# Kernel tuning notes

Hardware: AMD Instinct MI355X
Metric: run time of the kernel (lower is better)

Reference implementation:

```python
import jax, jax.numpy as jnp
import numpy as np

N, C, H, W = 8, 256, 64, 64
Q_REDUCE, K_REDUCE, V_REDUCE = 8, 8, 1


def setup_inputs() -> dict:
    key = jax.random.key(0)
    ks = jax.random.split(key, 6)
    Cq, Ck, Cv = C // Q_REDUCE, C // K_REDUCE, C // V_REDUCE
    s = 0.02
    x = jax.random.normal(ks[0], (N, C, H, W), dtype=jnp.float32)
    Wq = jax.random.normal(ks[1], (Cq, C), dtype=jnp.float32) * s
    Wk = jax.random.normal(ks[2], (Ck, C), dtype=jnp.float32) * s
    Wv = jax.random.normal(ks[3], (Cv, C), dtype=jnp.float32) * s
    Wo = jax.random.normal(ks[4], (C, Cv), dtype=jnp.float32) * s
    gamma = jax.random.normal(ks[5], (), dtype=jnp.float32)  # trained scalar (init 0.0 in torch)
    return {"x": x, "Wq": Wq, "Wk": Wk, "Wv": Wv, "Wo": Wo, "gamma": gamma}


def reference(x, Wq, Wk, Wv, Wo, gamma):
    n, c, h, w = x.shape
    xf = x.reshape(n, c, h * w)                      # [N, C, HW]
    q = jnp.einsum('qc,ncl->nql', Wq, xf)            # [N, Cq, HW] (1x1 conv)
    k = jnp.einsum('kc,ncl->nkl', Wk, xf)            # [N, Ck, HW]
    v = jnp.einsum('vc,ncl->nvl', Wv, xf)            # [N, Cv, HW]
    e = jnp.einsum('nci,ncj->nij', q, k)             # [N, HW, HW], unscaled energies
    a = jax.nn.softmax(e, axis=-1)                   # softmax over keys j
    o = jnp.einsum('nvi,nij->nvj', v, a)             # [N, Cv, HW]  (o = bmm(v, a))
    o = o.reshape(n, -1, w, h)                       # faithful: view(N,-1,W,H)
    out = jnp.einsum('ov,nvhw->nohw', Wo, o)         # output 1x1 conv
    return gamma * out
```

## Files before the change

kernel.cpp:

```cpp
#include <hip/hip_runtime.h>
#include <hip/hip_bf16.h>

#define NB 8
#define CIN 256
#define LL 4096
#define CQ 32
#define CV 256

typedef __attribute__((ext_vector_type(8))) short bf16x8;
typedef __attribute__((ext_vector_type(4))) float f32x4;

__device__ __forceinline__ unsigned short f2bf(float f) {
    union { __hip_bfloat16 h; unsigned short u; } c;
    c.h = __float2bfloat16(f);
    return c.u;
}
__device__ __forceinline__ unsigned int f2bf2(float a, float b) {
    union { __hip_bfloat162 h; unsigned int u; } c;
    float2 f; f.x = a; f.y = b;
    c.h = __float22bfloat162_rn(f);
    return c.u;
}

__global__ __launch_bounds__(256) void k_wcast(
    const float* __restrict__ Wq, const float* __restrict__ Wk,
    const float* __restrict__ Wv, const float* __restrict__ Wo,
    unsigned short* __restrict__ Wb, unsigned short* __restrict__ Wob)
{
    const float LOG2E = 1.4426950408889634f;
    const int row = blockIdx.x, t = threadIdx.x;
    if (row < 320) {
        float val;
        if (row < 32)      val = Wq[row * 256 + t] * LOG2E;
        else if (row < 64) val = Wk[(row - 32) * 256 + t];
        else               val = Wv[(row - 64) * 256 + t];
        Wb[row * 256 + t] = f2bf(val);
    } else {
        const int r2 = row - 320;
        Wob[r2 * 256 + t] = f2bf(Wo[r2 * 256 + t]);
    }
}

__global__ __launch_bounds__(256) void k_qkv2(
    const float* __restrict__ x, const unsigned short* __restrict__ Wb,
    unsigned short* __restrict__ qkt, unsigned short* __restrict__ v)
{
    __shared__ unsigned short xlds[64][264];
    __shared__ unsigned short tr[64][72];
    const int n = blockIdx.y, l0 = blockIdx.x * 64, t = threadIdx.x;
    const int w = t >> 6, lane = t & 63, lid = lane & 15, quad = lane >> 4;

    #pragma unroll
    for (int part = 0; part < 8; part++) {
        const int cbase = part * 32 + w * 8;
        float tmp[8];
        #pragma unroll
        for (int cc = 0; cc < 8; cc++)
            tmp[cc] = x[(n * CIN + cbase + cc) * LL + l0 + lane];
        bf16x8 s;
        #pragma unroll
        for (int cc = 0; cc < 8; cc++) s[cc] = (short)f2bf(tmp[cc]);
        *(bf16x8*)&xlds[lane][cbase] = s;
    }
    __syncthreads();

    const f32x4 fzero = {0.f, 0.f, 0.f, 0.f};
    f32x4 acc[5][4];
    #pragma unroll
    for (int mt = 0; mt < 5; mt++)
        #pragma unroll
        for (int nt = 0; nt < 4; nt++) acc[mt][nt] = fzero;

    for (int k0 = 0; k0 < 256; k0 += 32) {
        bf16x8 bx[4];
        #pragma unroll
        for (int nt = 0; nt < 4; nt++)
            bx[nt] = *(const bf16x8*)&xlds[nt * 16 + lid][k0 + quad * 8];
        #pragma unroll
        for (int mt = 0; mt < 5; mt++) {
            const int row = (mt == 0) ? (w * 16 + lid) : (64 + w * 64 + (mt - 1) * 16 + lid);
            const bf16x8 wa = *(const bf16x8*)&Wb[row * 256 + k0 + quad * 8];
            #pragma unroll
            for (int nt = 0; nt < 4; nt++)
                acc[mt][nt] = __builtin_amdgcn_mfma_f32_16x16x32_bf16(wa, bx[nt], acc[mt][nt], 0, 0, 0);
        }
    }
    #pragma unroll
    for (int mt = 1; mt < 5; mt++)
        #pragma unroll
        for (int nt = 0; nt < 4; nt++)
            #pragma unroll
            for (int reg = 0; reg < 4; reg++) {
                const int vr = w * 64 + (mt - 1) * 16 + quad * 4 + reg;
                v[((size_t)n * CV + vr) * LL + l0 + nt * 16 + lid] = f2bf(acc[mt][nt][reg]);
            }
    #pragma unroll
    for (int nt = 0; nt < 4; nt++)
        #pragma unroll
        for (int reg = 0; reg < 4; reg++)
            tr[nt * 16 + lid][w * 16 + quad * 4 + reg] = f2bf(acc[0][nt][reg]);
    __syncthreads();
    {
        const int l = t >> 2, c = (t & 3) * 16;
        uint4 d0 = *(const uint4*)&tr[l][c];
        uint4 d1 = *(const uint4*)&tr[l][c + 8];
        uint4* dst = (uint4*)&qkt[((size_t)n * LL + l0 + l) * 64 + c];
        dst[0] = d0; dst[1] = d1;
    }
}

__global__ __launch_bounds__(256) void k_rowsum2(
    const unsigned short* __restrict__ qkt, float* __restrict__ lns)
{
    __shared__ float red[64];
    const int n = blockIdx.y, i0 = blockIdx.x * 64, t = threadIdx.x;
    const int w = t >> 6, lane = t & 63, lid = lane & 15, quad = lane >> 4;
    if (t < 64) red[t] = 0.f;
    __syncthreads();

    bf16x8 aq[4];
    #pragma unroll
    for (int mt = 0; mt < 4; mt++)
        aq[mt] = *(const bf16x8*)&qkt[((size_t)n * LL + i0 + mt * 16 + lid) * 64 + quad * 8];

    const f32x4 fzero = {0.f, 0.f, 0.f, 0.f};
    float sums[4][4];
    #pragma unroll
    for (int mt = 0; mt < 4; mt++)
        #pragma unroll
        for (int reg = 0; reg < 4; reg++) sums[mt][reg] = 0.f;

    for (int jt = 0; jt < 16; jt++) {
        const int j0 = jt * 256 + w * 64;
        bf16x8 bk[4];
        #pragma unroll
        for (int nt = 0; nt < 4; nt++)
            bk[nt] = *(const bf16x8*)&qkt[((size_t)n * LL + j0 + nt * 16 + lid) * 64 + 32 + quad * 8];
        #pragma unroll
        for (int mt = 0; mt < 4; mt++)
            #pragma unroll
            for (int nt = 0; nt < 4; nt++) {
                f32x4 e = __builtin_amdgcn_mfma_f32_16x16x32_bf16(aq[mt], bk[nt], fzero, 0, 0, 0);
                sums[mt][0] += __builtin_exp2f(e[0]);
                sums[mt][1] += __builtin_exp2f(e[1]);
                sums[mt][2] += __builtin_exp2f(e[2]);
                sums[mt][3] += __builtin_exp2f(e[3]);
            }
    }
    #pragma unroll
    for (int mt = 0; mt < 4; mt++)
        #pragma unroll
        for (int reg = 0; reg < 4; reg++) {
            float s = sums[mt][reg];
            s += __shfl_xor(s, 1); s += __shfl_xor(s, 2);
            s += __shfl_xor(s, 4); s += __shfl_xor(s, 8);
            if (lid == 0) atomicAdd(&red[mt * 16 + quad * 4 + reg], s);
        }
    __syncthreads();
    if (t < 64) lns[n * LL + i0 + t] = -__builtin_log2f(red[t]);
}

__device__ __forceinline__ void write_p(unsigned short (*pl)[64], const f32x4* e,
                                        int w, int lid, int quad, int xkey)
{
    #pragma unroll
    for (int nt = 0; nt < 4; nt++) {
        const unsigned a01 = f2bf2(__builtin_exp2f(e[nt][0]), __builtin_exp2f(e[nt][1]));
        const unsigned a23 = f2bf2(__builtin_exp2f(e[nt][2]), __builtin_exp2f(e[nt][3]));
        const int chunk = (2 * w + (quad >> 1)) ^ xkey;
        unsigned* p = (unsigned*)&pl[nt * 16 + lid][chunk * 8 + (quad & 1) * 4];
        p[0] = a01; p[1] = a23;
    }
}

__global__ __launch_bounds__(256) void k_attn3(
    const unsigned short* __restrict__ qkt, const unsigned short* __restrict__ v,
    const float* __restrict__ lns, unsigned short* __restrict__ o)
{
    __shared__ unsigned short plds[2][64][64];
    const int n = blockIdx.y, j0 = blockIdx.x * 64, t = threadIdx.x;
    const int w = t >> 6, lane = t & 63, lid = lane & 15, quad = lane >> 4;
    const int xkey = lid & 7;

    const unsigned short* qrow = qkt + ((size_t)n * LL + w * 16 + lid) * 64 + quad * 8;
    const float* lrow = lns + (size_t)n * LL + w * 16 + quad * 4;
    const unsigned short* vrow = v + ((size_t)n * CV + w * 64 + lid) * LL + quad * 8;

    bf16x8 bk[4];
    #pragma unroll
    for (int nt = 0; nt < 4; nt++)
        bk[nt] = *(const bf16x8*)&qkt[((size_t)n * LL + j0 + nt * 16 + lid) * 64 + 32 + quad * 8];

    const f32x4 fzero = {0.f, 0.f, 0.f, 0.f};
    f32x4 acc[4][4];
    #pragma unroll
    for (int mt = 0; mt < 4; mt++)
        #pragma unroll
        for (int nt = 0; nt < 4; nt++) acc[mt][nt] = fzero;

    bf16x8 aq = *(const bf16x8*)qrow;
    f32x4 lnsC = *(const f32x4*)lrow;
    {
        f32x4 e[4];
        #pragma unroll
        for (int nt = 0; nt < 4; nt++)
            e[nt] = __builtin_amdgcn_mfma_f32_16x16x32_bf16(aq, bk[nt], lnsC, 0, 0, 0);
        aq = *(const bf16x8*)(qrow + (size_t)64 * 64);
        lnsC = *(const f32x4*)(lrow + 64);
        write_p(plds[0], e, w, lid, quad, xkey);
    }
    bf16x8 av[8];
    #pragma unroll
    for (int h = 0; h < 2; h++)
        #pragma unroll
        for (int mt = 0; mt < 4; mt++)
            av[h * 4 + mt] = *(const bf16x8*)(vrow + (size_t)mt * 16 * LL + h * 32);
    __syncthreads();

    for (int ic = 0; ic < 63; ic++) {
        const int cur = ic & 1;
        const size_t i0 = (size_t)ic * 64;
        f32x4 e2[4];
        #pragma unroll
        for (int nt = 0; nt < 4; nt++)
            e2[nt] = __builtin_amdgcn_mfma_f32_16x16x32_bf16(aq, bk[nt], lnsC, 0, 0, 0);
        const size_t ipf = (ic < 62) ? (i0 + 128) : i0;
        aq = *(const bf16x8*)(qrow + ipf * 64);
        lnsC = *(const f32x4*)(lrow + ipf);
        #pragma unroll
        for (int h = 0; h < 2; h++) {
            bf16x8 bp[4];
            #pragma unroll
            for (int nt = 0; nt < 4; nt++)
                bp[nt] = *(const bf16x8*)&plds[cur][nt * 16 + lid][((4 * h + quad) ^ xkey) * 8];
            #pragma unroll
            for (int mt = 0; mt < 4; mt++)
                #pragma unroll
                for (int nt = 0; nt < 4; nt++)
                    acc[mt][nt] = __builtin_amdgcn_mfma_f32_16x16x32_bf16(av[h * 4 + mt], bp[nt], acc[mt][nt], 0, 0, 0);
        }
        #pragma unroll
        for (int h = 0; h < 2; h++)
            #pragma unroll
            for (int mt = 0; mt < 4; mt++)
                av[h * 4 + mt] = *(const bf16x8*)(vrow + (size_t)mt * 16 * LL + (i0 + 64) + h * 32);
        write_p(plds[cur ^ 1], e2, w, lid, quad, xkey);
        __syncthreads();
    }
    #pragma unroll
    for (int h = 0; h < 2; h++) {
        bf16x8 bp[4];
        #pragma unroll
        for (int nt = 0; nt < 4; nt++)
            bp[nt] = *(const bf16x8*)&plds[1][nt * 16 + lid][((4 * h + quad) ^ xkey) * 8];
        #pragma unroll
        for (int mt = 0; mt < 4; mt++)
            #pragma unroll
            for (int nt = 0; nt < 4; nt++)
                acc[mt][nt] = __builtin_amdgcn_mfma_f32_16x16x32_bf16(av[h * 4 + mt], bp[nt], acc[mt][nt], 0, 0, 0);
    }
    #pragma unroll
    for (int mt = 0; mt < 4; mt++)
        #pragma unroll
        for (int nt = 0; nt < 4; nt++)
            #pragma unroll
            for (int reg = 0; reg < 4; reg++)
                o[((size_t)n * CV + w * 64 + mt * 16 + quad * 4 + reg) * LL + j0 + nt * 16 + lid] =
                    f2bf(acc[mt][nt][reg]);
}

__global__ __launch_bounds__(256) void k_out2(
    const unsigned short* __restrict__ o, const unsigned short* __restrict__ Wob,
    const float* __restrict__ gp, float* __restrict__ out)
{
    __shared__ unsigned short olds[64][264];
    const int n = blockIdx.y, l0 = blockIdx.x * 64, t = threadIdx.x;
    const int w = t >> 6, lane = t & 63, lid = lane & 15, quad = lane >> 4;

    #pragma unroll
    for (int part = 0; part < 8; part++) {
        const int cbase = part * 32 + w * 8;
        bf16x8 s;
        #pragma unroll
        for (int cc = 0; cc < 8; cc++)
            s[cc] = (short)o[((size_t)n * CV + cbase + cc) * LL + l0 + lane];
        *(bf16x8*)&olds[lane][cbase] = s;
    }
    __syncthreads();

    const f32x4 fzero = {0.f, 0.f, 0.f, 0.f};
    f32x4 acc[4][4];
    #pragma unroll
    for (int mt = 0; mt < 4; mt++)
        #pragma unroll
        for (int nt = 0; nt < 4; nt++) acc[mt][nt] = fzero;

    for (int k0 = 0; k0 < 256; k0 += 32) {
        bf16x8 bo[4];
        #pragma unroll
        for (int nt = 0; nt < 4; nt++)
            bo[nt] = *(const bf16x8*)&olds[nt * 16 + lid][k0 + quad * 8];
        #pragma unroll
        for (int mt = 0; mt < 4; mt++) {
            const bf16x8 wa = *(const bf16x8*)&Wob[(w * 64 + mt * 16 + lid) * 256 + k0 + quad * 8];
            #pragma unroll
            for (int nt = 0; nt < 4; nt++)
                acc[mt][nt] = __builtin_amdgcn_mfma_f32_16x16x32_bf16(wa, bo[nt], acc[mt][nt], 0, 0, 0);
        }
    }
    const float g = *gp;
    #pragma unroll
    for (int mt = 0; mt < 4; mt++)
        #pragma unroll
        for (int nt = 0; nt < 4; nt++)
            #pragma unroll
            for (int reg = 0; reg < 4; reg++) {
                const int r = w * 64 + mt * 16 + quad * 4 + reg;
                out[((size_t)n * CIN + r) * LL + l0 + nt * 16 + lid] = g * acc[mt][nt][reg];
            }
}

extern "C" void kernel_launch(void* const* d_in, const int* in_sizes, int n_in,
                              void* d_out, int out_size, void* d_ws, size_t ws_size,
                              hipStream_t stream) {
    const float* x     = (const float*)d_in[0];
    const float* Wq    = (const float*)d_in[1];
    const float* Wk    = (const float*)d_in[2];
    const float* Wv    = (const float*)d_in[3];
    const float* Wo    = (const float*)d_in[4];
    const float* gamma = (const float*)d_in[5];

    unsigned short* qkt = (unsigned short*)d_ws;
    unsigned short* v   = qkt + (size_t)NB * LL * 64;
    unsigned short* o   = v + (size_t)NB * CV * LL;
    unsigned short* Wb  = o + (size_t)NB * CV * LL;
    unsigned short* Wob = Wb + 320 * 256;
    float* lns          = (float*)(Wob + 256 * 256);
    float* out = (float*)d_out;

    k_wcast  <<<dim3(576),   256, 0, stream>>>(Wq, Wk, Wv, Wo, Wb, Wob);
    k_qkv2   <<<dim3(64, 8), 256, 0, stream>>>(x, Wb, qkt, v);
    k_rowsum2<<<dim3(64, 8), 256, 0, stream>>>(qkt, lns);
    k_attn3  <<<dim3(64, 8), 256, 0, stream>>>(qkt, v, lns, o);
    k_out2   <<<dim3(64, 8), 256, 0, stream>>>(o, Wob, gamma, out);
}
```

Measured before the change: 297.9 us.

## Fuse output projection into attention kernel and widen blocks to 512 threads

Folds the output 1x1 conv into the attention kernel, so the bf16 o tensor no longer goes to global memory and comes back in a separate kernel. The attention result is staged in shared memory and multiplied by Wo in place. All main kernels move to 512-thread blocks with 8 waves, and the attention loop now handles 128 query rows per step, with the P write moved ahead of the MFMA. The grid is linearised with batch as the fastest-varying index, which changes how blocks are scheduled across CUs. The trade-off is more shared memory and register pressure per block, which may reduce occupancy.

```diff
diff --git a/kernel.cpp b/kernel.cpp
--- a/kernel.cpp
+++ b/kernel.cpp
@@ -41,7 +41,7 @@
     }
 }
 
-__global__ __launch_bounds__(256) void k_qkv2(
+__global__ __launch_bounds__(512) void k_qkv3(
     const float* __restrict__ x, const unsigned short* __restrict__ Wb,
     unsigned short* __restrict__ qkt, unsigned short* __restrict__ v)
 {
@@ -51,12 +51,12 @@
     const int w = t >> 6, lane = t & 63, lid = lane & 15, quad = lane >> 4;
 
     #pragma unroll
-    for (int part = 0; part < 8; part++) {
-        const int cbase = part * 32 + w * 8;
+    for (int part = 0; part < 4; part++) {
+        const int cbase = part * 64 + w * 8;
         float tmp[8];
         #pragma unroll
         for (int cc = 0; cc < 8; cc++)
-            tmp[cc] = x[(n * CIN + cbase + cc) * LL + l0 + lane];
+            tmp[cc] = x[((size_t)n * CIN + cbase + cc) * LL + l0 + lane];
         bf16x8 s;
         #pragma unroll
         for (int cc = 0; cc < 8; cc++) s[cc] = (short)f2bf(tmp[cc]);
@@ -65,9 +65,9 @@
     __syncthreads();
 
     const f32x4 fzero = {0.f, 0.f, 0.f, 0.f};
-    f32x4 acc[5][4];
-    #pragma unroll
-    for (int mt = 0; mt < 5; mt++)
+    f32x4 acc[3][4];
+    #pragma unroll
+    for (int mt = 0; mt < 3; mt++)
         #pragma unroll
         for (int nt = 0; nt < 4; nt++) acc[mt][nt] = fzero;
 
@@ -77,44 +77,48 @@
         for (int nt = 0; nt < 4; nt++)
             bx[nt] = *(const bf16x8*)&xlds[nt * 16 + lid][k0 + quad * 8];
         #pragma unroll
-        for (int mt = 0; mt < 5; mt++) {
-            const int row = (mt == 0) ? (w * 16 + lid) : (64 + w * 64 + (mt - 1) * 16 + lid);
-            const bf16x8 wa = *(const bf16x8*)&Wb[row * 256 + k0 + quad * 8];
-            #pragma unroll
-            for (int nt = 0; nt < 4; nt++)
-                acc[mt][nt] = __builtin_amdgcn_mfma_f32_16x16x32_bf16(wa, bx[nt], acc[mt][nt], 0, 0, 0);
-        }
-    }
-    #pragma unroll
-    for (int mt = 1; mt < 5; mt++)
+        for (int vt = 0; vt < 2; vt++) {
+            const bf16x8 wa = *(const bf16x8*)&Wb[(64 + w * 32 + vt * 16 + lid) * 256 + k0 + quad * 8];
+            #pragma unroll
+            for (int nt = 0; nt < 4; nt++)
+                acc[vt][nt] = __builtin_amdgcn_mfma_f32_16x16x32_bf16(wa, bx[nt], acc[vt][nt], 0, 0, 0);
+        }
+        if (w < 4) {
+            const bf16x8 wa = *(const bf16x8*)&Wb[(w * 16 + lid) * 256 + k0 + quad * 8];
+            #pragma unroll
+            for (int nt = 0; nt < 4; nt++)
+                acc[2][nt] = __builtin_amdgcn_mfma_f32_16x16x32_bf16(wa, bx[nt], acc[2][nt], 0, 0, 0);
+        }
+    }
+    #pragma unroll
+    for (int vt = 0; vt < 2; vt++)
         #pragma unroll
         for (int nt = 0; nt < 4; nt++)
             #pragma unroll
             for (int reg = 0; reg < 4; reg++) {
-                const int vr = w * 64 + (mt - 1) * 16 + quad * 4 + reg;
-                v[((size_t)n * CV + vr) * LL + l0 + nt * 16 + lid] = f2bf(acc[mt][nt][reg]);
+                const int vr = w * 32 + vt * 16 + quad * 4 + reg;
+                v[((size_t)n * CV + vr) * LL + l0 + nt * 16 + lid] = f2bf(acc[vt][nt][reg]);
             }
-    #pragma unroll
-    for (int nt = 0; nt < 4; nt++)
-        #pragma unroll
-        for (int reg = 0; reg < 4; reg++)
-            tr[nt * 16 + lid][w * 16 + quad * 4 + reg] = f2bf(acc[0][nt][reg]);
+    if (w < 4) {
+        #pragma unroll
+        for (int nt = 0; nt < 4; nt++)
+            #pragma unroll
+            for (int reg = 0; reg < 4; reg++)
+                tr[nt * 16 + lid][w * 16 + quad * 4 + reg] = f2bf(acc[2][nt][reg]);
+    }
     __syncthreads();
     {
-        const int l = t >> 2, c = (t & 3) * 16;
-        uint4 d0 = *(const uint4*)&tr[l][c];
-        uint4 d1 = *(const uint4*)&tr[l][c + 8];
-        uint4* dst = (uint4*)&qkt[((size_t)n * LL + l0 + l) * 64 + c];
-        dst[0] = d0; dst[1] = d1;
-    }
-}
-
-__global__ __launch_bounds__(256) void k_rowsum2(
+        const int l = t >> 3, c = (t & 7) * 8;
+        *(uint4*)&qkt[((size_t)n * LL + l0 + l) * 64 + c] = *(const uint4*)&tr[l][c];
+    }
+}
+
+__global__ __launch_bounds__(512) void k_rowsum3(
     const unsigned short* __restrict__ qkt, float* __restrict__ lns)
 {
     __shared__ float red[64];
     const int n = blockIdx.y, i0 = blockIdx.x * 64, t = threadIdx.x;
-    const int w = t >> 6, lane = t & 63, lid = lane & 15, quad = lane >> 4;
+    const int w = t >> 6, lid = t & 15, quad = (t & 63) >> 4;
     if (t < 64) red[t] = 0.f;
     __syncthreads();
 
@@ -130,8 +134,8 @@
         #pragma unroll
         for (int reg = 0; reg < 4; reg++) sums[mt][reg] = 0.f;
 
-    for (int jt = 0; jt < 16; jt++) {
-        const int j0 = jt * 256 + w * 64;
+    for (int jt = 0; jt < 8; jt++) {
+        const int j0 = jt * 512 + w * 64;
         bf16x8 bk[4];
         #pragma unroll
         for (int nt = 0; nt < 4; nt++)
@@ -157,34 +161,39 @@
             if (lid == 0) atomicAdd(&red[mt * 16 + quad * 4 + reg], s);
         }
     __syncthreads();
-    if (t < 64) lns[n * LL + i0 + t] = -__builtin_log2f(red[t]);
-}
-
-__device__ __forceinline__ void write_p(unsigned short (*pl)[64], const f32x4* e,
+    if (t < 64) lns[(size_t)n * LL + i0 + t] = -__builtin_log2f(red[t]);
+}
+
+__device__ __forceinline__ void write_p(unsigned short (*pl)[128], const f32x4* e,
                                         int w, int lid, int quad, int xkey)
 {
+    const int chunk = (2 * w + (quad >> 1)) ^ xkey;
     #pragma unroll
     for (int nt = 0; nt < 4; nt++) {
         const unsigned a01 = f2bf2(__builtin_exp2f(e[nt][0]), __builtin_exp2f(e[nt][1]));
         const unsigned a23 = f2bf2(__builtin_exp2f(e[nt][2]), __builtin_exp2f(e[nt][3]));
-        const int chunk = (2 * w + (quad >> 1)) ^ xkey;
         unsigned* p = (unsigned*)&pl[nt * 16 + lid][chunk * 8 + (quad & 1) * 4];
         p[0] = a01; p[1] = a23;
     }
 }
 
-__global__ __launch_bounds__(256) void k_attn3(
+__global__ __launch_bounds__(512, 4) void k_attn4(
     const unsigned short* __restrict__ qkt, const unsigned short* __restrict__ v,
-    const float* __restrict__ lns, unsigned short* __restrict__ o)
-{
-    __shared__ unsigned short plds[2][64][64];
-    const int n = blockIdx.y, j0 = blockIdx.x * 64, t = threadIdx.x;
+    const float* __restrict__ lns, const unsigned short* __restrict__ Wob,
+    const float* __restrict__ gp, float* __restrict__ out)
+{
+    __shared__ unsigned short lraw[64 * 264];
+    unsigned short (*plds)[64][128] = (unsigned short (*)[64][128])lraw;
+    unsigned short (*olds)[264] = (unsigned short (*)[264])lraw;
+
+    const int bid = blockIdx.x;
+    const int n = bid & 7, j0 = (bid >> 3) * 64, t = threadIdx.x;
     const int w = t >> 6, lane = t & 63, lid = lane & 15, quad = lane >> 4;
     const int xkey = lid & 7;
 
     const unsigned short* qrow = qkt + ((size_t)n * LL + w * 16 + lid) * 64 + quad * 8;
     const float* lrow = lns + (size_t)n * LL + w * 16 + quad * 4;
-    const unsigned short* vrow = v + ((size_t)n * CV + w * 64 + lid) * LL + quad * 8;
+    const unsigned short* vrow = v + ((size_t)n * CV + w * 32 + lid) * LL + quad * 8;
 
     bf16x8 bk[4];
     #pragma unroll
@@ -192,9 +201,9 @@
         bk[nt] = *(const bf16x8*)&qkt[((size_t)n * LL + j0 + nt * 16 + lid) * 64 + 32 + quad * 8];
 
     const f32x4 fzero = {0.f, 0.f, 0.f, 0.f};
-    f32x4 acc[4][4];
-    #pragma unroll
-    for (int mt = 0; mt < 4; mt++)
+    f32x4 acc[2][4];
+    #pragma unroll
+    for (int mt = 0; mt < 2; mt++)
         #pragma unroll
         for (int nt = 0; nt < 4; nt++) acc[mt][nt] = fzero;
 
@@ -205,118 +214,99 @@
         #pragma unroll
         for (int nt = 0; nt < 4; nt++)
             e[nt] = __builtin_amdgcn_mfma_f32_16x16x32_bf16(aq, bk[nt], lnsC, 0, 0, 0);
-        aq = *(const bf16x8*)(qrow + (size_t)64 * 64);
-        lnsC = *(const f32x4*)(lrow + 64);
+        aq = *(const bf16x8*)(qrow + (size_t)128 * 64);
+        lnsC = *(const f32x4*)(lrow + 128);
         write_p(plds[0], e, w, lid, quad, xkey);
     }
     bf16x8 av[8];
     #pragma unroll
-    for (int h = 0; h < 2; h++)
-        #pragma unroll
-        for (int mt = 0; mt < 4; mt++)
-            av[h * 4 + mt] = *(const bf16x8*)(vrow + (size_t)mt * 16 * LL + h * 32);
-    __syncthreads();
-
-    for (int ic = 0; ic < 63; ic++) {
+    for (int mt = 0; mt < 2; mt++)
+        #pragma unroll
+        for (int h = 0; h < 4; h++)
+            av[mt * 4 + h] = *(const bf16x8*)(vrow + (size_t)mt * 16 * LL + h * 32);
+    __syncthreads();
+
+    for (int ic = 0; ic < 31; ic++) {
         const int cur = ic & 1;
-        const size_t i0 = (size_t)ic * 64;
+        const size_t i0 = (size_t)ic * 128;
         f32x4 e2[4];
         #pragma unroll
         for (int nt = 0; nt < 4; nt++)
             e2[nt] = __builtin_amdgcn_mfma_f32_16x16x32_bf16(aq, bk[nt], lnsC, 0, 0, 0);
-        const size_t ipf = (ic < 62) ? (i0 + 128) : i0;
+        const size_t ipf = (ic < 30) ? (i0 + 256) : i0;
         aq = *(const bf16x8*)(qrow + ipf * 64);
         lnsC = *(const f32x4*)(lrow + ipf);
-        #pragma unroll
-        for (int h = 0; h < 2; h++) {
+        write_p(plds[cur ^ 1], e2, w, lid, quad, xkey);
+        #pragma unroll
+        for (int h = 0; h < 4; h++) {
             bf16x8 bp[4];
             #pragma unroll
             for (int nt = 0; nt < 4; nt++)
                 bp[nt] = *(const bf16x8*)&plds[cur][nt * 16 + lid][((4 * h + quad) ^ xkey) * 8];
             #pragma unroll
-            for (int mt = 0; mt < 4; mt++)
+            for (int mt = 0; mt < 2; mt++)
                 #pragma unroll
                 for (int nt = 0; nt < 4; nt++)
-                    acc[mt][nt] = __builtin_amdgcn_mfma_f32_16x16x32_bf16(av[h * 4 + mt], bp[nt], acc[mt][nt], 0, 0, 0);
-        }
-        #pragma unroll
-        for (int h = 0; h < 2; h++)
-            #pragma unroll
-            for (int mt = 0; mt < 4; mt++)
-                av[h * 4 + mt] = *(const bf16x8*)(vrow + (size_t)mt * 16 * LL + (i0 + 64) + h * 32);
-        write_p(plds[cur ^ 1], e2, w, lid, quad, xkey);
+                    acc[mt][nt] = __builtin_amdgcn_mfma_f32_16x16x32_bf16(av[mt * 4 + h], bp[nt], acc[mt][nt], 0, 0, 0);
+        }
+        #pragma unroll
+        for (int mt = 0; mt < 2; mt++)
+            #pragma unroll
+            for (int h = 0; h < 4; h++)
+                av[mt * 4 + h] = *(const bf16x8*)(vrow + (size_t)mt * 16 * LL + (i0 + 128) + h * 32);
         __syncthreads();
     }
     #pragma unroll
-    for (int h = 0; h < 2; h++) {
+    for (int h = 0; h < 4; h++) {
         bf16x8 bp[4];
         #pragma unroll
         for (int nt = 0; nt < 4; nt++)
             bp[nt] = *(const bf16x8*)&plds[1][nt * 16 + lid][((4 * h + quad) ^ xkey) * 8];
         #pragma unroll
-        for (int mt = 0; mt < 4; mt++)
-            #pragma unroll
-            for (int nt = 0; nt < 4; nt++)
-                acc[mt][nt] = __builtin_amdgcn_mfma_f32_16x16x32_bf16(av[h * 4 + mt], bp[nt], acc[mt][nt], 0, 0, 0);
-    }
-    #pragma unroll
-    for (int mt = 0; mt < 4; mt++)
-        #pragma unroll
-        for (int nt = 0; nt < 4; nt++)
-            #pragma unroll
-            for (int reg = 0; reg < 4; reg++)
-                o[((size_t)n * CV + w * 64 + mt * 16 + quad * 4 + reg) * LL + j0 + nt * 16 + lid] =
-                    f2bf(acc[mt][nt][reg]);
-}
-
-__global__ __launch_bounds__(256) void k_out2(
-    const unsigned short* __restrict__ o, const unsigned short* __restrict__ Wob,
-    const float* __restrict__ gp, float* __restrict__ out)
-{
-    __shared__ unsigned short olds[64][264];
-    const int n = blockIdx.y, l0 = blockIdx.x * 64, t = threadIdx.x;
-    const int w = t >> 6, lane = t & 63, lid = lane & 15, quad = lane >> 4;
-
-    #pragma unroll
-    for (int part = 0; part < 8; part++) {
-        const int cbase = part * 32 + w * 8;
-        bf16x8 s;
-        #pragma unroll
-        for (int cc = 0; cc < 8; cc++)
-            s[cc] = (short)o[((size_t)n * CV + cbase + cc) * LL + l0 + lane];
-        *(bf16x8*)&olds[lane][cbase] = s;
-    }
-    __syncthreads();
-
-    const f32x4 fzero = {0.f, 0.f, 0.f, 0.f};
-    f32x4 acc[4][4];
-    #pragma unroll
-    for (int mt = 0; mt < 4; mt++)
-        #pragma unroll
-        for (int nt = 0; nt < 4; nt++) acc[mt][nt] = fzero;
-
+        for (int mt = 0; mt < 2; mt++)
+            #pragma unroll
+            for (int nt = 0; nt < 4; nt++)
+                acc[mt][nt] = __builtin_amdgcn_mfma_f32_16x16x32_bf16(av[mt * 4 + h], bp[nt], acc[mt][nt], 0, 0, 0);
+    }
+    __syncthreads();
+
+    #pragma unroll
+    for (int mt = 0; mt < 2; mt++)
+        #pragma unroll
+        for (int nt = 0; nt < 4; nt++) {
+            ushort4 s;
+            s.x = f2bf(acc[mt][nt][0]); s.y = f2bf(acc[mt][nt][1]);
+            s.z = f2bf(acc[mt][nt][2]); s.w = f2bf(acc[mt][nt][3]);
+            *(ushort4*)&olds[nt * 16 + lid][w * 32 + mt * 16 + quad * 4] = s;
+        }
+    __syncthreads();
+    f32x4 oacc[2][4];
+    #pragma unroll
+    for (int mt = 0; mt < 2; mt++)
+        #pragma unroll
+        for (int nt = 0; nt < 4; nt++) oacc[mt][nt] = fzero;
     for (int k0 = 0; k0 < 256; k0 += 32) {
         bf16x8 bo[4];
         #pragma unroll
         for (int nt = 0; nt < 4; nt++)
             bo[nt] = *(const bf16x8*)&olds[nt * 16 + lid][k0 + quad * 8];
         #pragma unroll
-        for (int mt = 0; mt < 4; mt++) {
-            const bf16x8 wa = *(const bf16x8*)&Wob[(w * 64 + mt * 16 + lid) * 256 + k0 + quad * 8];
-            #pragma unroll
-            for (int nt = 0; nt < 4; nt++)
-                acc[mt][nt] = __builtin_amdgcn_mfma_f32_16x16x32_bf16(wa, bo[nt], acc[mt][nt], 0, 0, 0);
+        for (int mt = 0; mt < 2; mt++) {
+            const bf16x8 wa = *(const bf16x8*)&Wob[(w * 32 + mt * 16 + lid) * 256 + k0 + quad * 8];
+            #pragma unroll
+            for (int nt = 0; nt < 4; nt++)
+                oacc[mt][nt] = __builtin_amdgcn_mfma_f32_16x16x32_bf16(wa, bo[nt], oacc[mt][nt], 0, 0, 0);
         }
     }
     const float g = *gp;
     #pragma unroll
-    for (int mt = 0; mt < 4; mt++)
+    for (int mt = 0; mt < 2; mt++)
         #pragma unroll
         for (int nt = 0; nt < 4; nt++)
             #pragma unroll
             for (int reg = 0; reg < 4; reg++) {
-                const int r = w * 64 + mt * 16 + quad * 4 + reg;
-                out[((size_t)n * CIN + r) * LL + l0 + nt * 16 + lid] = g * acc[mt][nt][reg];
+                const int r = w * 32 + mt * 16 + quad * 4 + reg;
+                out[((size_t)n * CIN + r) * LL + j0 + nt * 16 + lid] = g * oacc[mt][nt][reg];
             }
 }
 
@@ -332,15 +322,13 @@
 
     unsigned short* qkt = (unsigned short*)d_ws;
     unsigned short* v   = qkt + (size_t)NB * LL * 64;
-    unsigned short* o   = v + (size_t)NB * CV * LL;
-    unsigned short* Wb  = o + (size_t)NB * CV * LL;
+    unsigned short* Wb  = v + (size_t)NB * CV * LL;
     unsigned short* Wob = Wb + 320 * 256;
     float* lns          = (float*)(Wob + 256 * 256);
     float* out = (float*)d_out;
 
     k_wcast  <<<dim3(576),   256, 0, stream>>>(Wq, Wk, Wv, Wo, Wb, Wob);
-    k_qkv2   <<<dim3(64, 8), 256, 0, stream>>>(x, Wb, qkt, v);
-    k_rowsum2<<<dim3(64, 8), 256, 0, stream>>>(qkt, lns);
-    k_attn3  <<<dim3(64, 8), 256, 0, stream>>>(qkt, v, lns, o);
-    k_out2   <<<dim3(64, 8), 256, 0, stream>>>(o, Wob, gamma, out);
-}
+    k_qkv3   <<<dim3(64, 8), 512, 0, stream>>>(x, Wb, qkt, v);
+    k_rowsum3<<<dim3(64, 8), 512, 0, stream>>>(qkt, lns);
+    k_attn4  <<<dim3(512),   512, 0, stream>>>(qkt, v, lns, Wob, gamma, out);
+}
```

Result: faster. 289.3 us (-2.9%).
